# Optimization experiments

Hardware: AMD Instinct MI355X
Metric: run time of the kernel (lower is better)

## Reference

```python
import jax, jax.numpy as jnp
from jax import lax
import numpy as np

# ---- static config derived from init_kwargs ----
BATCH, SEQ, DM = 16, 1024, 512
EXPAND, DSTATE, DCONV, HEADDIM = 2, 64, 4, 64
DIN = EXPAND * DM                 # 1024 (d_inner)
NH = DIN // HEADDIM               # 16 heads
CONVDIM = DIN + 2 * DSTATE        # 1152 (x, B, C share depthwise conv)
DINPROJ = 2 * DIN + 2 * DSTATE + NH  # 2192
IN_CH, OUT_CH = SEQ, 1024         # Conv1d sees (B, L, d_model) as (N, C=L, len=d_model)
EPS = 1e-5


def setup_inputs() -> dict:
    key = jax.random.key(0)
    ks = jax.random.split(key, 8)
    sc = lambda k, shape, s=0.02: jax.random.normal(k, shape, jnp.float32) * s
    return {
        "x": jax.random.normal(ks[0], (BATCH, SEQ, DM), jnp.float32),
        # Mamba2 params (bias=False for in/out proj by default)
        "in_proj_w": sc(ks[1], (DINPROJ, DM)),
        "conv1d_w": sc(ks[2], (CONVDIM, DCONV), 0.1),   # depthwise kernel
        "conv1d_b": jnp.zeros((CONVDIM,), jnp.float32),
        "dt_bias": sc(ks[3], (NH,), 0.1),
        "A_log": jnp.log(jnp.linspace(1.0, 16.0, NH, dtype=jnp.float32)),
        "D": jnp.ones((NH,), jnp.float32),
        "rms_w": jnp.ones((DIN,), jnp.float32),
        "out_proj_w": sc(ks[4], (DM, DIN)),
        # trailing Conv1d(in_channels=SEQ, out_channels, k=3, pad=1)
        "conv_w": sc(ks[5], (OUT_CH, IN_CH, 3)),
        "conv_b": jnp.zeros((OUT_CH,), jnp.float32),
        # BatchNorm1d affine params (training-mode batch stats)
        "bn_gamma": jnp.ones((OUT_CH,), jnp.float32),
        "bn_beta": jnp.zeros((OUT_CH,), jnp.float32),
    }


def _mamba2(u, in_proj_w, conv1d_w, conv1d_b, dt_bias, A_log, D, rms_w, out_proj_w):
    B, L, _ = u.shape
    zxbcdt = u @ in_proj_w.T                          # (B, L, DINPROJ)
    z = zxbcdt[..., :DIN]
    xBC = zxbcdt[..., DIN:DIN + CONVDIM]
    dt = zxbcdt[..., DIN + CONVDIM:]                  # (B, L, NH)
    dt = jax.nn.softplus(dt + dt_bias)

    # causal depthwise conv over time + SiLU
    xBC_t = jnp.pad(xBC.transpose(0, 2, 1), ((0, 0), (0, 0), (DCONV - 1, 0)))
    xBC_c = lax.conv_general_dilated(
        xBC_t, conv1d_w[:, None, :], (1,), 'VALID',
        dimension_numbers=('NCH', 'OIH', 'NCH'), feature_group_count=CONVDIM)
    xBC = jax.nn.silu(xBC_c + conv1d_b[None, :, None]).transpose(0, 2, 1)  # (B, L, CONVDIM)

    x_in = xBC[..., :DIN].reshape(B, L, NH, HEADDIM)  # (B, L, H, P)
    Bm = xBC[..., DIN:DIN + DSTATE]                   # (B, L, N), ngroups=1
    Cm = xBC[..., DIN + DSTATE:]                      # (B, L, N)

    A = -jnp.exp(A_log)                               # (H,)
    dA = jnp.exp(dt * A)                              # (B, L, H)

    def step(h, inp):
        dA_t, dt_t, x_t, B_t, C_t = inp
        h = h * dA_t[:, :, None, None] + jnp.einsum('bh,bhp,bn->bhpn', dt_t, x_t, B_t)
        y_t = jnp.einsum('bhpn,bn->bhp', h, C_t)
        return h, y_t

    h0 = jnp.zeros((B, NH, HEADDIM, DSTATE), u.dtype)
    xs = (dA.transpose(1, 0, 2), dt.transpose(1, 0, 2),
          x_in.transpose(1, 0, 2, 3), Bm.transpose(1, 0, 2), Cm.transpose(1, 0, 2))
    _, ys = lax.scan(step, h0, xs)                    # (L, B, H, P)
    y = ys.transpose(1, 0, 2, 3) + D[None, None, :, None] * x_in
    y = y.reshape(B, L, DIN)

    # gated RMSNorm: norm(y * silu(z))
    y = y * jax.nn.silu(z)
    y = y * lax.rsqrt(jnp.mean(y * y, axis=-1, keepdims=True) + EPS) * rms_w
    return y @ out_proj_w.T                           # (B, L, DM)


def reference(x, in_proj_w, conv1d_w, conv1d_b, dt_bias, A_log, D, rms_w,
              out_proj_w, conv_w, conv_b, bn_gamma, bn_beta):
    u = _mamba2(x, in_proj_w, conv1d_w, conv1d_b, dt_bias, A_log, D, rms_w, out_proj_w)
    # Conv1d over (N, C=SEQ, len=DM), kernel 3, padding 1
    c = lax.conv_general_dilated(u, conv_w, (1,), [(1, 1)],
                                 dimension_numbers=('NCH', 'OIH', 'NCH'))
    c = c + conv_b[None, :, None]                     # (B, OUT_CH, DM)
    # BatchNorm1d (training-mode batch statistics, biased variance)
    mean = jnp.mean(c, axis=(0, 2), keepdims=True)
    var = jnp.mean((c - mean) ** 2, axis=(0, 2), keepdims=True)
    c = (c - mean) * lax.rsqrt(var + EPS)
    c = c * bn_gamma[None, :, None] + bn_beta[None, :, None]
    return jax.nn.silu(c)
```

## Files before the change

kernel.cpp:

```cpp
#include <hip/hip_runtime.h>
#include <hip/hip_bf16.h>

#define BATCH 16
#define SEQ   1024
#define DM    512
#define DSTATE 64
#define DIN   1024
#define NH    16
#define CONVDIM 1152
#define DINPROJ 2192
#define NPAD  2304
#define XDTW  1280
#define OC    1024
#define EPSF  1e-5f

typedef __attribute__((ext_vector_type(8))) short short8;
typedef __attribute__((ext_vector_type(4))) float f32x4;

__device__ __forceinline__ void g2lds16(const __hip_bfloat16* g, __hip_bfloat16* l) {
  __builtin_amdgcn_global_load_lds(
      (const __attribute__((address_space(1))) void*)g,
      (__attribute__((address_space(3))) void*)l, 16, 0, 0);
}

__device__ __forceinline__ float siluf(float x) { return x / (1.f + expf(-x)); }
__device__ __forceinline__ float b2f(unsigned short u) {
  return __uint_as_float(((unsigned int)u) << 16);
}
__device__ __forceinline__ unsigned short f2b(float v) {
  __hip_bfloat16 h = __float2bfloat16(v);
  return __builtin_bit_cast(unsigned short, h);
}

__global__ __launch_bounds__(256) void gemm1_kernel(
    const __hip_bfloat16* __restrict__ A,
    const __hip_bfloat16* __restrict__ B,
    __hip_bfloat16* __restrict__ zbuf,
    __hip_bfloat16* __restrict__ xdt)
{
  __shared__ __hip_bfloat16 sAB[2][2][8192];
  const int tid  = threadIdx.x;
  const int lane = tid & 63;
  const int wid  = tid >> 6;
  const int wr = wid >> 1, wc = wid & 1;
  const long row0 = (long)blockIdx.x * 128;
  const int  col0 = blockIdx.y * 128;
  const __hip_bfloat16* Ab = A + row0 * 512;
  const __hip_bfloat16* Bb = B + (long)col0 * 512;

  auto stage = [&](int kt, int buf) {
#pragma unroll
    for (int it = 0; it < 4; ++it) {
      int idx = it * 256 + tid;
      int r = idx >> 3;
      int kk = (idx & 7) << 3;
      g2lds16(Ab + (long)r * 512 + kt + kk, &sAB[buf][0][idx * 8]);
      g2lds16(Bb + (long)r * 512 + kt + kk, &sAB[buf][1][idx * 8]);
    }
  };

  f32x4 acc[4][4] = {};
  stage(0, 0);
  __syncthreads();
  int cur = 0;
  for (int kt = 0; kt < 512; kt += 64) {
    if (kt + 64 < 512) stage(kt + 64, cur ^ 1);
    const __hip_bfloat16* sA = &sAB[cur][0][0];
    const __hip_bfloat16* sB = &sAB[cur][1][0];
#pragma unroll
    for (int kk = 0; kk < 64; kk += 32) {
      const int kl = kk + (lane >> 4) * 8;
      short8 af[4], bfr[4];
#pragma unroll
      for (int m = 0; m < 4; ++m)
        af[m] = *(const short8*)(sA + (wr * 64 + m * 16 + (lane & 15)) * 64 + kl);
#pragma unroll
      for (int n = 0; n < 4; ++n)
        bfr[n] = *(const short8*)(sB + (wc * 64 + n * 16 + (lane & 15)) * 64 + kl);
#pragma unroll
      for (int m = 0; m < 4; ++m)
#pragma unroll
        for (int n = 0; n < 4; ++n)
          acc[m][n] = __builtin_amdgcn_mfma_f32_16x16x32_bf16(af[m], bfr[n], acc[m][n], 0, 0, 0);
    }
    __syncthreads();
    cur ^= 1;
  }

  __hip_bfloat16* Cb;
  int ldc, coff;
  if (col0 < 1024) { Cb = zbuf; ldc = 1024; coff = col0; }
  else             { Cb = xdt;  ldc = XDTW; coff = col0 - 1024; }
  const int rb = (int)row0 + wr * 64 + ((lane >> 4) << 2);
  const int cb = coff + wc * 64 + (lane & 15);
#pragma unroll
  for (int m = 0; m < 4; ++m)
#pragma unroll
    for (int n = 0; n < 4; ++n) {
      const int r = rb + m * 16, cc = cb + n * 16;
#pragma unroll
      for (int q = 0; q < 4; ++q)
        Cb[(long)(r + q) * ldc + cc] = __float2bfloat16(acc[m][n][q]);
    }
}

__global__ __launch_bounds__(256) void gemm2_trans_kernel(
    const __hip_bfloat16* __restrict__ A,
    const __hip_bfloat16* __restrict__ B,
    const float* __restrict__ rn,
    __hip_bfloat16* __restrict__ uTp)
{
  __shared__ unsigned short smem[2][2][8192];
  const int tid  = threadIdx.x;
  const int lane = tid & 63;
  const int wid  = tid >> 6;
  const int wr = wid >> 1, wc = wid & 1;
  const long row0 = (long)blockIdx.x * 128;
  const int  col0 = blockIdx.y * 128;
  const int  b  = (int)(row0 >> 10);
  const int  l0 = (int)(row0 & 1023);
  const __hip_bfloat16* Ab = A + row0 * 1024;
  const __hip_bfloat16* Bb = B + (long)col0 * 1024;

  auto stage = [&](int kt, int buf) {
#pragma unroll
    for (int it = 0; it < 4; ++it) {
      int idx = it * 256 + tid;
      int r = idx >> 3;
      int kk = (idx & 7) << 3;
      g2lds16(Ab + (long)r * 1024 + kt + kk, (__hip_bfloat16*)&smem[buf][0][idx * 8]);
      g2lds16(Bb + (long)r * 1024 + kt + kk, (__hip_bfloat16*)&smem[buf][1][idx * 8]);
    }
  };

  f32x4 acc[4][4] = {};
  stage(0, 0);
  __syncthreads();
  int cur = 0;
  for (int kt = 0; kt < 1024; kt += 64) {
    if (kt + 64 < 1024) stage(kt + 64, cur ^ 1);
    const __hip_bfloat16* sA = (const __hip_bfloat16*)&smem[cur][0][0];
    const __hip_bfloat16* sB = (const __hip_bfloat16*)&smem[cur][1][0];
#pragma unroll
    for (int kk = 0; kk < 64; kk += 32) {
      const int kl = kk + (lane >> 4) * 8;
      short8 af[4], bfr[4];
#pragma unroll
      for (int m = 0; m < 4; ++m)
        af[m] = *(const short8*)(sA + (wr * 64 + m * 16 + (lane & 15)) * 64 + kl);
#pragma unroll
      for (int n = 0; n < 4; ++n)
        bfr[n] = *(const short8*)(sB + (wc * 64 + n * 16 + (lane & 15)) * 64 + kl);
#pragma unroll
      for (int m = 0; m < 4; ++m)
#pragma unroll
        for (int n = 0; n < 4; ++n)
          acc[m][n] = __builtin_amdgcn_mfma_f32_16x16x32_bf16(af[m], bfr[n], acc[m][n], 0, 0, 0);
    }
    __syncthreads();
    cur ^= 1;
  }

  unsigned short* sT = &smem[0][0][0];
  const int rl = wr * 64 + ((lane >> 4) << 2);
  const int cl = wc * 64 + (lane & 15);
#pragma unroll
  for (int m = 0; m < 4; ++m) {
    float rnv[4];
#pragma unroll
    for (int q = 0; q < 4; ++q) rnv[q] = rn[row0 + rl + m * 16 + q];
#pragma unroll
    for (int n = 0; n < 4; ++n) {
      const int c = cl + n * 16;
#pragma unroll
      for (int q = 0; q < 4; ++q)
        sT[c * 128 + rl + m * 16 + q] = f2b(acc[m][n][q] * rnv[q]);
    }
  }
  __syncthreads();

  unsigned short* up = (unsigned short*)uTp + (long)b * 514 * 1024;
  const int w = tid >> 6;
#pragma unroll
  for (int k = 0; k < 32; ++k) {
    const int row = w * 32 + k;
    ushort2 o2;
    o2.x = sT[row * 128 + lane * 2];
    o2.y = sT[row * 128 + lane * 2 + 1];
    *(ushort2*)(up + (long)(col0 + row + 1) * 1024 + l0 + lane * 2) = o2;
  }
}

__global__ __launch_bounds__(256) void gemm_conv_kernel(
    const __hip_bfloat16* __restrict__ A,
    const __hip_bfloat16* __restrict__ uTp,
    __hip_bfloat16* __restrict__ C)
{
  const int f = blockIdx.x + 8 * (blockIdx.y + 4 * blockIdx.z);
  const int g = (f & 7) * 64 + (f >> 3);
  const int bx = g & 7, by = (g >> 3) & 3, bz = g >> 5;

  __shared__ __hip_bfloat16 sAB[2][2][8192];
  const int tid  = threadIdx.x;
  const int lane = tid & 63;
  const int wid  = tid >> 6;
  const int wr = wid >> 1, wc = wid & 1;
  const int row0 = bx * 128;
  const int col0 = by * 128;
  const __hip_bfloat16* Ab = A + (long)row0 * 3072;
  const __hip_bfloat16* Ub = uTp + (long)bz * 514 * 1024;

  auto stage = [&](int kt, int buf) {
    const int seg = kt >> 10;
    const int io  = kt & 1023;
#pragma unroll
    for (int it = 0; it < 4; ++it) {
      int idx = it * 256 + tid;
      int r = idx >> 3;
      int kk = (idx & 7) << 3;
      g2lds16(Ab + (long)r * 3072 + kt + kk, &sAB[buf][0][idx * 8]);
      g2lds16(Ub + (long)(col0 + r + seg) * 1024 + io + kk, &sAB[buf][1][idx * 8]);
    }
  };

  f32x4 acc[4][4] = {};
  stage(0, 0);
  __syncthreads();
  int cur = 0;
  for (int kt = 0; kt < 3072; kt += 64) {
    if (kt + 64 < 3072) stage(kt + 64, cur ^ 1);
    const __hip_bfloat16* sA = &sAB[cur][0][0];
    const __hip_bfloat16* sB = &sAB[cur][1][0];
#pragma unroll
    for (int kk = 0; kk < 64; kk += 32) {
      const int kl = kk + (lane >> 4) * 8;
      short8 af[4], bfr[4];
#pragma unroll
      for (int m = 0; m < 4; ++m)
        af[m] = *(const short8*)(sA + (wr * 64 + m * 16 + (lane & 15)) * 64 + kl);
#pragma unroll
      for (int n = 0; n < 4; ++n)
        bfr[n] = *(const short8*)(sB + (wc * 64 + n * 16 + (lane & 15)) * 64 + kl);
#pragma unroll
      for (int m = 0; m < 4; ++m)
#pragma unroll
        for (int n = 0; n < 4; ++n)
          acc[m][n] = __builtin_amdgcn_mfma_f32_16x16x32_bf16(af[m], bfr[n], acc[m][n], 0, 0, 0);
    }
    __syncthreads();
    cur ^= 1;
  }

  __hip_bfloat16* Cb = C + (long)bz * OC * DM;
  const int rb = row0 + wr * 64 + ((lane >> 4) << 2);
  const int cb = col0 + wc * 64 + (lane & 15);
#pragma unroll
  for (int m = 0; m < 4; ++m)
#pragma unroll
    for (int n = 0; n < 4; ++n) {
      const int r = rb + m * 16, cc = cb + n * 16;
#pragma unroll
      for (int q = 0; q < 4; ++q)
        Cb[(long)(r + q) * DM + cc] = __float2bfloat16(acc[m][n][q]);
    }
}

__global__ __launch_bounds__(256) void fill_kernel(float* __restrict__ out, float v, long n) {
  long i = (long)blockIdx.x * 256 + threadIdx.x;
  if (i < n) out[i] = v;
}

__global__ __launch_bounds__(256) void prep_kernel(
    const float* __restrict__ x, const float* __restrict__ w1,
    const float* __restrict__ w2, const float* __restrict__ rms_w,
    const float* __restrict__ w3,
    __hip_bfloat16* __restrict__ xbf, __hip_bfloat16* __restrict__ w1b,
    __hip_bfloat16* __restrict__ w2b, __hip_bfloat16* __restrict__ w3b,
    float* __restrict__ rnacc)
{
  const int bid = blockIdx.x;
  if (bid < 8192) {
    long i = (long)bid * 256 + threadIdx.x;
    float4 v = *(const float4*)(x + i * 4);
    __hip_bfloat16* o = xbf + i * 4;
    o[0] = __float2bfloat16(v.x);
    o[1] = __float2bfloat16(v.y);
    o[2] = __float2bfloat16(v.z);
    o[3] = __float2bfloat16(v.w);
  } else if (bid < 12800) {
    int i = (bid - 8192) * 256 + threadIdx.x;
    int r = i >> 9;
    w1b[i] = (r < DINPROJ) ? __float2bfloat16(w1[i]) : __float2bfloat16(0.f);
  } else if (bid < 13312) {
    int i = (bid - 12800) * 256 + threadIdx.x;
    float4 v = *(const float4*)(w2 + (long)i * 4);
    float4 gw = *(const float4*)(rms_w + ((i * 4) & 1023));
    __hip_bfloat16* o = w2b + (long)i * 4;
    o[0] = __float2bfloat16(v.x * gw.x);
    o[1] = __float2bfloat16(v.y * gw.y);
    o[2] = __float2bfloat16(v.z * gw.z);
    o[3] = __float2bfloat16(v.w * gw.w);
  } else if (bid < 17408) {
    int t = (bid - 13312) * 256 + threadIdx.x;
    int o = t >> 10, i = t & 1023;
    const float* p = w3 + (long)o * 3072 + i * 3;
    __hip_bfloat16* q = w3b + (long)o * 3072 + i;
    q[0]    = __float2bfloat16(p[0]);
    q[1024] = __float2bfloat16(p[1]);
    q[2048] = __float2bfloat16(p[2]);
  } else {
    int i = (bid - 17408) * 256 + threadIdx.x;
    rnacc[i] = 0.f;
  }
}

__global__ __launch_bounds__(256) void conv1d_slide_kernel(
    const __hip_bfloat16* __restrict__ xdt, const float* __restrict__ cw,
    const float* __restrict__ cb, const float* __restrict__ dt_bias,
    __hip_bfloat16* __restrict__ xbc, float* __restrict__ dtb)
{
  const int pair = blockIdx.x * 256 + threadIdx.x;
  const int c = pair * 2;
  if (c >= CONVDIM + NH) return;
  const int b  = blockIdx.z;
  const int l0 = blockIdx.y * 16;
  const long rowb = (long)b * SEQ;
  const unsigned short* src = (const unsigned short*)xdt + rowb * XDTW + c;

  if (c < CONVDIM) {
    const float4 wa = *(const float4*)(cw + c * 4);
    const float4 wb = *(const float4*)(cw + (c + 1) * 4);
    const float ba = cb[c], bb = cb[c + 1];
    float w0x, w0y, w1x, w1y, w2x, w2y;
    {
      ushort2 v;
      if (l0 >= 3) { v = *(const ushort2*)(src + (long)(l0 - 3) * XDTW); w0x = b2f(v.x); w0y = b2f(v.y); }
      else { w0x = 0.f; w0y = 0.f; }
      if (l0 >= 2) { v = *(const ushort2*)(src + (long)(l0 - 2) * XDTW); w1x = b2f(v.x); w1y = b2f(v.y); }
      else { w1x = 0.f; w1y = 0.f; }
      if (l0 >= 1) { v = *(const ushort2*)(src + (long)(l0 - 1) * XDTW); w2x = b2f(v.x); w2y = b2f(v.y); }
      else { w2x = 0.f; w2y = 0.f; }
    }
    unsigned short* dst = (unsigned short*)xbc + rowb * CONVDIM + c;
#pragma unroll
    for (int i = 0; i < 16; ++i) {
      const int l = l0 + i;
      const ushort2 v = *(const ushort2*)(src + (long)l * XDTW);
      const float xv0 = b2f(v.x), xv1 = b2f(v.y);
      float a0 = ba, a1 = bb;
      a0 += w0x * wa.x; a1 += w0y * wb.x;
      a0 += w1x * wa.y; a1 += w1y * wb.y;
      a0 += w2x * wa.z; a1 += w2y * wb.z;
      a0 += xv0 * wa.w; a1 += xv1 * wb.w;
      ushort2 o;
      o.x = f2b(siluf(a0));
      o.y = f2b(siluf(a1));
      *(ushort2*)(dst + (long)l * CONVDIM) = o;
      w0x = w1x; w0y = w1y; w1x = w2x; w1y = w2y; w2x = xv0; w2y = xv1;
    }
  } else {
    const int hh = c - CONVDIM;
    const float b0 = dt_bias[hh], b1 = dt_bias[hh + 1];
#pragma unroll
    for (int i = 0; i < 16; ++i) {
      const long l = l0 + i;
      const ushort2 v = *(const ushort2*)(src + l * XDTW);
      const float d0 = b2f(v.x) + b0, d1 = b2f(v.y) + b1;
      float2 o;
      o.x = fmaxf(d0, 0.f) + log1pf(expf(-fabsf(d0)));
      o.y = fmaxf(d1, 0.f) + log1pf(expf(-fabsf(d1)));
      *(float2*)(dtb + (rowb + l) * NH + hh) = o;
    }
  }
}

__global__ __launch_bounds__(256) void ssd_chunk_kernel(
    const __hip_bfloat16* __restrict__ xbc, const float* __restrict__ dtb,
    const float* __restrict__ A_log, __hip_bfloat16* __restrict__ ypre,
    __hip_bfloat16* __restrict__ Tbuf, float* __restrict__ Aprod)
{
  const int c = blockIdx.x, h = blockIdx.y, b = blockIdx.z;
  const int tid = threadIdx.x, lane = tid & 63, wid = tid >> 6;
  const int wr = wid >> 1, wc = wid & 1;
  const long r0 = (long)b * SEQ + c * 64;

  __shared__ unsigned short sB[64 * 72], sC[64 * 72], sXT[64 * 72],
                            sBwT[64 * 72], sM[64 * 72];
  __shared__ float sS[64], sDt[64];

  {
    const int j = tid >> 2, seg = (tid & 3) * 16;
    const unsigned short* row = (const unsigned short*)(xbc + (r0 + j) * CONVDIM);
    short8 v0 = *(const short8*)(row + DIN + seg);
    short8 v1 = *(const short8*)(row + DIN + seg + 8);
    *(short8*)&sB[j * 72 + seg] = v0;
    *(short8*)&sB[j * 72 + seg + 8] = v1;
    v0 = *(const short8*)(row + DIN + DSTATE + seg);
    v1 = *(const short8*)(row + DIN + DSTATE + seg + 8);
    *(short8*)&sC[j * 72 + seg] = v0;
    *(short8*)&sC[j * 72 + seg + 8] = v1;
    short8 x0 = *(const short8*)(row + h * 64 + seg);
    short8 x1 = *(const short8*)(row + h * 64 + seg + 8);
#pragma unroll
    for (int e = 0; e < 8; ++e) {
      sXT[(seg + e) * 72 + j] = (unsigned short)x0[e];
      sXT[(seg + 8 + e) * 72 + j] = (unsigned short)x1[e];
    }
  }
  if (tid < 64) {
    float dt = dtb[(r0 + tid) * NH + h];
    float s = -__expf(A_log[h]) * dt;
#pragma unroll
    for (int off = 1; off < 64; off <<= 1) {
      float o = __shfl_up(s, off);
      if (lane >= off) s += o;
    }
    sDt[tid] = dt;
    sS[tid] = s;
    if (tid == 63) Aprod[((b * 16 + h) * 16) + c] = __expf(s);
  }
  __syncthreads();

  {
    const int j = tid >> 2, n0 = (tid & 3) * 16;
    const float w = __expf(sS[63] - sS[j]) * sDt[j];
#pragma unroll
    for (int e = 0; e < 16; ++e)
      sBwT[(n0 + e) * 72 + j] = f2b(w * b2f(sB[j * 72 + n0 + e]));
  }
  {
    f32x4 acc1[2][2] = {};
#pragma unroll
    for (int kk = 0; kk < 64; kk += 32) {
      const int kl = kk + (lane >> 4) * 8;
      short8 af[2], bfr[2];
#pragma unroll
      for (int m = 0; m < 2; ++m)
        af[m] = *(const short8*)&sC[(wr * 32 + m * 16 + (lane & 15)) * 72 + kl];
#pragma unroll
      for (int n = 0; n < 2; ++n)
        bfr[n] = *(const short8*)&sB[(wc * 32 + n * 16 + (lane & 15)) * 72 + kl];
#pragma unroll
      for (int m = 0; m < 2; ++m)
#pragma unroll
        for (int n = 0; n < 2; ++n)
          acc1[m][n] = __builtin_amdgcn_mfma_f32_16x16x32_bf16(af[m], bfr[n], acc1[m][n], 0, 0, 0);
    }
    const int rq = (lane >> 4) * 4, cc = lane & 15;
#pragma unroll
    for (int m = 0; m < 2; ++m)
#pragma unroll
      for (int n = 0; n < 2; ++n)
#pragma unroll
        for (int q = 0; q < 4; ++q) {
          const int i = wr * 32 + m * 16 + rq + q;
          const int jj = wc * 32 + n * 16 + cc;
          float f = (jj <= i) ? __expf(sS[i] - sS[jj]) * sDt[jj] : 0.f;
          sM[i * 72 + jj] = f2b(acc1[m][n][q] * f);
        }
  }
  __syncthreads();

  f32x4 acc2[2][2] = {}, acc3[2][2] = {};
#pragma unroll
  for (int kk = 0; kk < 64; kk += 32) {
    const int kl = kk + (lane >> 4) * 8;
    short8 am[2], axB[2], axA[2], abw[2];
#pragma unroll
    for (int m = 0; m < 2; ++m) {
      am[m]  = *(const short8*)&sM[(wr * 32 + m * 16 + (lane & 15)) * 72 + kl];
      axA[m] = *(const short8*)&sXT[(wr * 32 + m * 16 + (lane & 15)) * 72 + kl];
    }
#pragma unroll
    for (int n = 0; n < 2; ++n) {
      axB[n] = *(const short8*)&sXT[(wc * 32 + n * 16 + (lane & 15)) * 72 + kl];
      abw[n] = *(const short8*)&sBwT[(wc * 32 + n * 16 + (lane & 15)) * 72 + kl];
    }
#pragma unroll
    for (int m = 0; m < 2; ++m)
#pragma unroll
      for (int n = 0; n < 2; ++n) {
        acc2[m][n] = __builtin_amdgcn_mfma_f32_16x16x32_bf16(am[m], axB[n], acc2[m][n], 0, 0, 0);
        acc3[m][n] = __builtin_amdgcn_mfma_f32_16x16x32_bf16(axA[m], abw[n], acc3[m][n], 0, 0, 0);
      }
  }
  __syncthreads();
  {
    const int rq = (lane >> 4) * 4, cc = lane & 15;
#pragma unroll
    for (int m = 0; m < 2; ++m)
#pragma unroll
      for (int n = 0; n < 2; ++n)
#pragma unroll
        for (int q = 0; q < 4; ++q) {
          const int i = wr * 32 + m * 16 + rq + q;
          const int pj = wc * 32 + n * 16 + cc;
          sM[i * 72 + pj]   = f2b(acc2[m][n][q]);
          sBwT[i * 72 + pj] = f2b(acc3[m][n][q]);
        }
  }
  __syncthreads();
  {
    const int j = tid >> 2, seg = (tid & 3) * 16;
    unsigned short* yp = (unsigned short*)ypre + (r0 + j) * DIN + h * 64 + seg;
    *(short8*)yp       = *(const short8*)&sM[j * 72 + seg];
    *(short8*)(yp + 8) = *(const short8*)&sM[j * 72 + seg + 8];
    const long tb = (((long)(b * 16 + h)) * 16 + c) * 4096;
    unsigned short* tp = (unsigned short*)Tbuf + tb + j * 64 + seg;
    *(short8*)tp       = *(const short8*)&sBwT[j * 72 + seg];
    *(short8*)(tp + 8) = *(const short8*)&sBwT[j * 72 + seg + 8];
  }
}

__global__ __launch_bounds__(1024) void ssd_state_kernel(
    __hip_bfloat16* __restrict__ Tbuf, const float* __restrict__ Aprod)
{
  const int bh = blockIdx.x;
  const int t = threadIdx.x;
  float h0 = 0.f, h1 = 0.f, h2 = 0.f, h3 = 0.f;
  unsigned short* base = (unsigned short*)Tbuf + (long)bh * 16 * 4096 + t * 4;
  for (int c = 0; c < 16; ++c) {
    unsigned short* p = base + (long)c * 4096;
    ushort4 tv = *(const ushort4*)p;
    ushort4 hv;
    hv.x = f2b(h0); hv.y = f2b(h1); hv.z = f2b(h2); hv.w = f2b(h3);
    *(ushort4*)p = hv;
    const float ap = Aprod[bh * 16 + c];
    h0 = h0 * ap + b2f(tv.x);
    h1 = h1 * ap + b2f(tv.y);
    h2 = h2 * ap + b2f(tv.z);
    h3 = h3 * ap + b2f(tv.w);
  }
}

__global__ __launch_bounds__(256) void ssd_out_kernel(
    const __hip_bfloat16* __restrict__ xbc, const float* __restrict__ dtb,
    const float* __restrict__ A_log, const __hip_bfloat16* __restrict__ Hbuf,
    const __hip_bfloat16* __restrict__ zbuf, const float* __restrict__ Dv,
    __hip_bfloat16* __restrict__ ypre, float* __restrict__ rnacc)
{
  const int c = blockIdx.x, h = blockIdx.y, b = blockIdx.z;
  const int tid = threadIdx.x, lane = tid & 63, wid = tid >> 6;
  const int wr = wid >> 1, wc = wid & 1;
  const long r0 = (long)b * SEQ + c * 64;

  __shared__ unsigned short sC[64 * 72], sH[64 * 72];
  __shared__ float sS[64];
  __shared__ float sRedW[2][64];

  {
    const int j = tid >> 2, seg = (tid & 3) * 16;
    const unsigned short* row = (const unsigned short*)(xbc + (r0 + j) * CONVDIM);
    short8 v0 = *(const short8*)(row + DIN + DSTATE + seg);
    short8 v1 = *(const short8*)(row + DIN + DSTATE + seg + 8);
    *(short8*)&sC[j * 72 + seg] = v0;
    *(short8*)&sC[j * 72 + seg + 8] = v1;
    const unsigned short* hrow =
        (const unsigned short*)Hbuf + (((long)(b * 16 + h)) * 16 + c) * 4096 + j * 64;
    v0 = *(const short8*)(hrow + seg);
    v1 = *(const short8*)(hrow + seg + 8);
    *(short8*)&sH[j * 72 + seg] = v0;
    *(short8*)&sH[j * 72 + seg + 8] = v1;
  }
  if (tid < 64) {
    float dt = dtb[(r0 + tid) * NH + h];
    float s = -__expf(A_log[h]) * dt;
#pragma unroll
    for (int off = 1; off < 64; off <<= 1) {
      float o = __shfl_up(s, off);
      if (lane >= off) s += o;
    }
    sS[tid] = s;
  }
  __syncthreads();

  f32x4 acc[2][2] = {};
#pragma unroll
  for (int kk = 0; kk < 64; kk += 32) {
    const int kl = kk + (lane >> 4) * 8;
    short8 af[2], bfr[2];
#pragma unroll
    for (int m = 0; m < 2; ++m)
      af[m] = *(const short8*)&sC[(wr * 32 + m * 16 + (lane & 15)) * 72 + kl];
#pragma unroll
    for (int n = 0; n < 2; ++n)
      bfr[n] = *(const short8*)&sH[(wc * 32 + n * 16 + (lane & 15)) * 72 + kl];
#pragma unroll
    for (int m = 0; m < 2; ++m)
#pragma unroll
      for (int n = 0; n < 2; ++n)
        acc[m][n] = __builtin_amdgcn_mfma_f32_16x16x32_bf16(af[m], bfr[n], acc[m][n], 0, 0, 0);
  }
  __syncthreads();
  const float Dh = Dv[h];
  const int rq = (lane >> 4) * 4, cc = lane & 15;
  float rsum[2][4] = {};
#pragma unroll
  for (int m = 0; m < 2; ++m)
#pragma unroll
    for (int n = 0; n < 2; ++n)
#pragma unroll
      for (int q = 0; q < 4; ++q) {
        const int i = wr * 32 + m * 16 + rq + q;
        const int p = wc * 32 + n * 16 + cc;
        const long r = r0 + i;
        const long oidx = r * DIN + h * 64 + p;
        float yv = b2f(((const unsigned short*)ypre)[oidx]);
        float xv = b2f(((const unsigned short*)xbc)[r * CONVDIM + h * 64 + p]);
        float zv = b2f(((const unsigned short*)zbuf)[r * DIN + h * 64 + p]);
        yv += __expf(sS[i]) * acc[m][n][q] + Dh * xv;
        const float g = yv * siluf(zv);
        rsum[m][q] += g * g;
        sC[i * 72 + p] = f2b(g);
      }
#pragma unroll
  for (int m = 0; m < 2; ++m)
#pragma unroll
    for (int q = 0; q < 4; ++q) {
      float v = rsum[m][q];
      v += __shfl_xor(v, 1);
      v += __shfl_xor(v, 2);
      v += __shfl_xor(v, 4);
      v += __shfl_xor(v, 8);
      if ((lane & 15) == 0)
        sRedW[wc][wr * 32 + m * 16 + rq + q] = v;
    }
  __syncthreads();
  {
    const int j = tid >> 2, seg = (tid & 3) * 16;
    unsigned short* yp = (unsigned short*)ypre + (r0 + j) * DIN + h * 64 + seg;
    *(short8*)yp       = *(const short8*)&sC[j * 72 + seg];
    *(short8*)(yp + 8) = *(const short8*)&sC[j * 72 + seg + 8];
  }
  if (tid < 64) atomicAdd(&rnacc[r0 + tid], sRedW[0][tid] + sRedW[1][tid]);
}

__global__ __launch_bounds__(256) void rnfin_pad_kernel(
    const float* __restrict__ rnacc, float* __restrict__ rn,
    __hip_bfloat16* __restrict__ uTp)
{
  const int bid = blockIdx.x;
  if (bid < 64) {
    int i = bid * 256 + threadIdx.x;
    rn[i] = rsqrtf(rnacc[i] * (1.f / DIN) + EPSF);
  } else {
    int t = (bid - 64) * 256 + threadIdx.x;
    int n = t >> 11, w = t & 2047;
    long row = (w >> 10) ? 513 : 0;
    uTp[(long)n * 514 * 1024 + row * 1024 + (w & 1023)] = __float2bfloat16(0.f);
  }
}

__global__ __launch_bounds__(256) void bn_stats_kernel(
    const __hip_bfloat16* __restrict__ c, float* __restrict__ stats)
{
  const int o = blockIdx.x, t = threadIdx.x;
  float s = 0.f, s2 = 0.f;
  for (int n = 0; n < BATCH; ++n) {
    const unsigned short* base = (const unsigned short*)c + ((long)n * OC + o) * DM;
    ushort2 v = *(const ushort2*)(base + t * 2);
    float a = b2f(v.x), bb = b2f(v.y);
    s += a + bb;
    s2 += a * a + bb * bb;
  }
#pragma unroll
  for (int m = 32; m >= 1; m >>= 1) { s += __shfl_xor(s, m); s2 += __shfl_xor(s2, m); }
  __shared__ float r1[4], r2[4];
  if ((t & 63) == 0) { r1[t >> 6] = s; r2[t >> 6] = s2; }
  __syncthreads();
  if (t == 0) {
    s = r1[0] + r1[1] + r1[2] + r1[3];
    s2 = r2[0] + r2[1] + r2[2] + r2[3];
    float mean = s * (1.f / 8192.f);
    float var = s2 * (1.f / 8192.f) - mean * mean;
    stats[o] = mean;
    stats[OC + o] = rsqrtf(var + EPSF);
  }
}

__global__ __launch_bounds__(256) void bn_silu_kernel(
    const __hip_bfloat16* __restrict__ c, const float* __restrict__ stats,
    const float* __restrict__ gamma, const float* __restrict__ beta,
    float* __restrict__ out)
{
  long gid = (long)blockIdx.x * 256 + threadIdx.x;
  long base = gid * 4;
  int o = (int)((base >> 9) & (OC - 1));
  float mean = stats[o], rstd = stats[OC + o];
  float g = gamma[o] * rstd;
  float sh = beta[o] - mean * g;
  ushort4 v = *(const ushort4*)((const unsigned short*)c + base);
  float4 r;
  r.x = siluf(b2f(v.x) * g + sh);
  r.y = siluf(b2f(v.y) * g + sh);
  r.z = siluf(b2f(v.z) * g + sh);
  r.w = siluf(b2f(v.w) * g + sh);
  *(float4*)(out + base) = r;
}

extern "C" void kernel_launch(void* const* d_in, const int* in_sizes, int n_in,
                              void* d_out, int out_size, void* d_ws, size_t ws_size,
                              hipStream_t stream) {
  const float* x         = (const float*)d_in[0];
  const float* in_projw  = (const float*)d_in[1];
  const float* conv1dw   = (const float*)d_in[2];
  const float* conv1db   = (const float*)d_in[3];
  const float* dt_bias   = (const float*)d_in[4];
  const float* A_log     = (const float*)d_in[5];
  const float* Dv        = (const float*)d_in[6];
  const float* rms_w     = (const float*)d_in[7];
  const float* out_projw = (const float*)d_in[8];
  const float* conv_w    = (const float*)d_in[9];
  const float* bn_gamma  = (const float*)d_in[11];
  const float* bn_beta   = (const float*)d_in[12];
  float* out = (float*)d_out;
  char* ws = (char*)d_ws;

  __hip_bfloat16* zbuf = (__hip_bfloat16*)(ws + 0UL);
  __hip_bfloat16* xdt  = (__hip_bfloat16*)(ws + 33554432UL);
  __hip_bfloat16* xbcb = (__hip_bfloat16*)(ws + 75497472UL);
  __hip_bfloat16* ypb  = (__hip_bfloat16*)(ws + 113246208UL);
  __hip_bfloat16* xbf  = (__hip_bfloat16*)(ws + 146800640UL);
  __hip_bfloat16* w1b  = (__hip_bfloat16*)(ws + 163577856UL);
  __hip_bfloat16* w2b  = (__hip_bfloat16*)(ws + 165937152UL);
  __hip_bfloat16* w3b  = (__hip_bfloat16*)(ws + 166985728UL);
  float* dtb           = (float*)(ws + 173277184UL);
  float* Aprod         = (float*)(ws + 174325760UL);
  float* stats         = (float*)(ws + 174342144UL);
  float* rn            = (float*)(ws + 174350336UL);
  float* rnacc         = (float*)(ws + 174415872UL);
  const size_t WS_NEED = 174481408UL;

  const long outn = (long)BATCH * OC * DM;
  if (ws_size < WS_NEED) {
    fill_kernel<<<(int)((outn + 255) / 256), 256, 0, stream>>>(out, (float)(ws_size >> 20), outn);
    return;
  }

  __hip_bfloat16* Tbuf = xdt;
  __hip_bfloat16* uTp  = xdt;
  __hip_bfloat16* cbuf = zbuf;

  prep_kernel<<<17472, 256, 0, stream>>>(x, in_projw, out_projw, rms_w, conv_w,
                                         xbf, w1b, w2b, w3b, rnacc);

  gemm1_kernel<<<dim3(128, 18), 256, 0, stream>>>(xbf, w1b, zbuf, xdt);
  conv1d_slide_kernel<<<dim3(3, 64, BATCH), 256, 0, stream>>>(xdt, conv1dw, conv1db,
                                                              dt_bias, xbcb, dtb);
  ssd_chunk_kernel<<<dim3(16, 16, 16), 256, 0, stream>>>(xbcb, dtb, A_log, ypb, Tbuf, Aprod);
  ssd_state_kernel<<<256, 1024, 0, stream>>>(Tbuf, Aprod);
  ssd_out_kernel<<<dim3(16, 16, 16), 256, 0, stream>>>(xbcb, dtb, A_log, Tbuf, zbuf,
                                                       Dv, ypb, rnacc);
  rnfin_pad_kernel<<<192, 256, 0, stream>>>(rnacc, rn, uTp);
  gemm2_trans_kernel<<<dim3(128, 4), 256, 0, stream>>>(ypb, w2b, rn, uTp);
  gemm_conv_kernel<<<dim3(8, 4, 16), 256, 0, stream>>>(w3b, uTp, cbuf);
  bn_stats_kernel<<<1024, 256, 0, stream>>>(cbuf, stats);
  bn_silu_kernel<<<8192, 256, 0, stream>>>(cbuf, stats, bn_gamma, bn_beta, out);
}
```

Measured before the change: 273.3 us.

## Split conv GEMM K-tile into halves with fine-grained vmcnt waits; vectorize w1 conversion

```diff
diff --git a/kernel.cpp b/kernel.cpp
--- a/kernel.cpp
+++ b/kernel.cpp
@@ -200,7 +200,7 @@
   const int g = (f & 7) * 64 + (f >> 3);
   const int bx = g & 7, by = (g >> 3) & 3, bz = g >> 5;
 
-  __shared__ __hip_bfloat16 sAB[2][2][8192];
+  __shared__ __hip_bfloat16 sAB[2][2][2][4096];
   const int tid  = threadIdx.x;
   const int lane = tid & 63;
   const int wid  = tid >> 6;
@@ -210,44 +210,62 @@
   const __hip_bfloat16* Ab = A + (long)row0 * 3072;
   const __hip_bfloat16* Ub = uTp + (long)bz * 514 * 1024;
 
-  auto stage = [&](int kt, int buf) {
+  auto stage_half = [&](int kt, int buf, int h) {
     const int seg = kt >> 10;
-    const int io  = kt & 1023;
-#pragma unroll
-    for (int it = 0; it < 4; ++it) {
+    const int io  = (kt & 1023) + h * 32;
+#pragma unroll
+    for (int it = 0; it < 2; ++it) {
       int idx = it * 256 + tid;
-      int r = idx >> 3;
-      int kk = (idx & 7) << 3;
-      g2lds16(Ab + (long)r * 3072 + kt + kk, &sAB[buf][0][idx * 8]);
-      g2lds16(Ub + (long)(col0 + r + seg) * 1024 + io + kk, &sAB[buf][1][idx * 8]);
+      int r = idx >> 2;
+      int kq = (idx & 3) << 3;
+      g2lds16(Ab + (long)r * 3072 + kt + h * 32 + kq, &sAB[buf][0][h][idx * 8]);
+      g2lds16(Ub + (long)(col0 + r + seg) * 1024 + io + kq, &sAB[buf][1][h][idx * 8]);
     }
   };
 
   f32x4 acc[4][4] = {};
-  stage(0, 0);
-  __syncthreads();
+  auto mfma_half = [&](int buf, int h) {
+    const int kl = (lane >> 4) * 8;
+    const __hip_bfloat16* sA = &sAB[buf][0][h][0];
+    const __hip_bfloat16* sB = &sAB[buf][1][h][0];
+    short8 af[4], bfr[4];
+#pragma unroll
+    for (int m = 0; m < 4; ++m)
+      af[m] = *(const short8*)(sA + (wr * 64 + m * 16 + (lane & 15)) * 32 + kl);
+#pragma unroll
+    for (int n = 0; n < 4; ++n)
+      bfr[n] = *(const short8*)(sB + (wc * 64 + n * 16 + (lane & 15)) * 32 + kl);
+#pragma unroll
+    for (int m = 0; m < 4; ++m)
+#pragma unroll
+      for (int n = 0; n < 4; ++n)
+        acc[m][n] = __builtin_amdgcn_mfma_f32_16x16x32_bf16(af[m], bfr[n], acc[m][n], 0, 0, 0);
+  };
+
+  stage_half(0, 0, 0);
+  stage_half(0, 0, 1);
   int cur = 0;
   for (int kt = 0; kt < 3072; kt += 64) {
-    if (kt + 64 < 3072) stage(kt + 64, cur ^ 1);
-    const __hip_bfloat16* sA = &sAB[cur][0][0];
-    const __hip_bfloat16* sB = &sAB[cur][1][0];
-#pragma unroll
-    for (int kk = 0; kk < 64; kk += 32) {
-      const int kl = kk + (lane >> 4) * 8;
-      short8 af[4], bfr[4];
-#pragma unroll
-      for (int m = 0; m < 4; ++m)
-        af[m] = *(const short8*)(sA + (wr * 64 + m * 16 + (lane & 15)) * 64 + kl);
-#pragma unroll
-      for (int n = 0; n < 4; ++n)
-        bfr[n] = *(const short8*)(sB + (wc * 64 + n * 16 + (lane & 15)) * 64 + kl);
-#pragma unroll
-      for (int m = 0; m < 4; ++m)
-#pragma unroll
-        for (int n = 0; n < 4; ++n)
-          acc[m][n] = __builtin_amdgcn_mfma_f32_16x16x32_bf16(af[m], bfr[n], acc[m][n], 0, 0, 0);
-    }
-    __syncthreads();
+    const bool nx = (kt + 64) < 3072;
+    if (nx) {
+      stage_half(kt + 64, cur ^ 1, 0);
+      asm volatile("s_waitcnt vmcnt(8)" ::: "memory");
+    } else {
+      asm volatile("s_waitcnt vmcnt(4)" ::: "memory");
+    }
+    __builtin_amdgcn_s_barrier();
+    __builtin_amdgcn_sched_barrier(0);
+    mfma_half(cur, 0);
+    if (nx) {
+      stage_half(kt + 64, cur ^ 1, 1);
+      asm volatile("s_waitcnt vmcnt(8)" ::: "memory");
+    } else {
+      asm volatile("s_waitcnt vmcnt(0)" ::: "memory");
+    }
+    __builtin_amdgcn_s_barrier();
+    __builtin_amdgcn_sched_barrier(0);
+    mfma_half(cur, 1);
+    __builtin_amdgcn_s_barrier();
     cur ^= 1;
   }
 
@@ -287,12 +305,19 @@
     o[1] = __float2bfloat16(v.y);
     o[2] = __float2bfloat16(v.z);
     o[3] = __float2bfloat16(v.w);
-  } else if (bid < 12800) {
+  } else if (bid < 9344) {
     int i = (bid - 8192) * 256 + threadIdx.x;
-    int r = i >> 9;
-    w1b[i] = (r < DINPROJ) ? __float2bfloat16(w1[i]) : __float2bfloat16(0.f);
-  } else if (bid < 13312) {
-    int i = (bid - 12800) * 256 + threadIdx.x;
+    int r = i >> 7;
+    float4 v;
+    if (r < DINPROJ) v = *(const float4*)(w1 + (long)i * 4);
+    else { v.x = 0.f; v.y = 0.f; v.z = 0.f; v.w = 0.f; }
+    __hip_bfloat16* o = w1b + (long)i * 4;
+    o[0] = __float2bfloat16(v.x);
+    o[1] = __float2bfloat16(v.y);
+    o[2] = __float2bfloat16(v.z);
+    o[3] = __float2bfloat16(v.w);
+  } else if (bid < 9856) {
+    int i = (bid - 9344) * 256 + threadIdx.x;
     float4 v = *(const float4*)(w2 + (long)i * 4);
     float4 gw = *(const float4*)(rms_w + ((i * 4) & 1023));
     __hip_bfloat16* o = w2b + (long)i * 4;
@@ -300,8 +325,8 @@
     o[1] = __float2bfloat16(v.y * gw.y);
     o[2] = __float2bfloat16(v.z * gw.z);
     o[3] = __float2bfloat16(v.w * gw.w);
-  } else if (bid < 17408) {
-    int t = (bid - 13312) * 256 + threadIdx.x;
+  } else if (bid < 13952) {
+    int t = (bid - 9856) * 256 + threadIdx.x;
     int o = t >> 10, i = t & 1023;
     const float* p = w3 + (long)o * 3072 + i * 3;
     __hip_bfloat16* q = w3b + (long)o * 3072 + i;
@@ -309,7 +334,7 @@
     q[1024] = __float2bfloat16(p[1]);
     q[2048] = __float2bfloat16(p[2]);
   } else {
-    int i = (bid - 17408) * 256 + threadIdx.x;
+    int i = (bid - 13952) * 256 + threadIdx.x;
     rnacc[i] = 0.f;
   }
 }
@@ -741,7 +766,7 @@
   __hip_bfloat16* uTp  = xdt;
   __hip_bfloat16* cbuf = zbuf;
 
-  prep_kernel<<<17472, 256, 0, stream>>>(x, in_projw, out_projw, rms_w, conv_w,
+  prep_kernel<<<14016, 256, 0, stream>>>(x, in_projw, out_projw, rms_w, conv_w,
                                          xbf, w1b, w2b, w3b, rnacc);
 
   gemm1_kernel<<<dim3(128, 18), 256, 0, stream>>>(xbf, w1b, zbuf, xdt);
```

Result: slower. 280.7 us (+2.7%).
